# Kernel tuning notes

Hardware: AMD Instinct MI355X
Metric: run time of the kernel (lower is better)

## Reference

```python
import jax, jax.numpy as jnp
import numpy as np
from jax import lax

B, T, N_INPUT = 64, 2048, 257
HIDDEN = 32
N_OUTPUT = 10


def setup_inputs() -> dict:
    key = jax.random.key(0)
    ks = jax.random.split(key, 7)
    return {
        "specs": jax.random.normal(ks[0], (B, T, N_INPUT), dtype=jnp.float32),
        "W_ih": jax.random.normal(ks[1], (4 * HIDDEN, N_INPUT), dtype=jnp.float32) * 0.05,
        "W_hh": jax.random.normal(ks[2], (4 * HIDDEN, HIDDEN), dtype=jnp.float32) * 0.05,
        "b_ih": jax.random.normal(ks[3], (4 * HIDDEN,), dtype=jnp.float32) * 0.05,
        "b_hh": jax.random.normal(ks[4], (4 * HIDDEN,), dtype=jnp.float32) * 0.05,
        "W_out": jax.random.normal(ks[5], (N_OUTPUT, HIDDEN), dtype=jnp.float32) * 0.05,
        "b_out": jax.random.normal(ks[6], (N_OUTPUT,), dtype=jnp.float32) * 0.05,
    }


def reference(specs, W_ih, W_hh, b_ih, b_hh, W_out, b_out):
    # specs: [B, T, n_input]. PyTorch LSTMCell, gate order (i, f, g, o).
    b, t, _ = specs.shape
    h0 = jnp.zeros((b, HIDDEN), dtype=specs.dtype)
    c0 = jnp.zeros((b, HIDDEN), dtype=specs.dtype)
    # Precompute input projection for all timesteps in one GEMM: [B, T, 4H]
    x_proj = jnp.einsum("bti,gi->btg", specs, W_ih) + b_ih + b_hh
    x_proj = jnp.swapaxes(x_proj, 0, 1)  # [T, B, 4H] for scan

    def step(carry, xg):
        h, c = carry
        gates = xg + h @ W_hh.T  # [B, 4H]
        i, f, g, o = jnp.split(gates, 4, axis=-1)
        i = jax.nn.sigmoid(i)
        f = jax.nn.sigmoid(f)
        g = jnp.tanh(g)
        o = jax.nn.sigmoid(o)
        c = f * c + i * g
        h = o * jnp.tanh(c)
        return (h, c), None

    (hn, _), _ = lax.scan(step, (h0, c0), x_proj)
    logits = jax.nn.relu(hn) @ W_out.T + b_out  # [B, n_output]
    return jax.nn.log_softmax(logits, axis=1)
```

## Files before the change

kernel.cpp:

```cpp
#include <hip/hip_runtime.h>

#define B_SZ 64
#define T_LEN 2048
#define NIN 257
#define HID 32
#define G4 128
#define NOUT 10

#define TBT 128
#define PAD 34
#define CH 8
#define NSCAN 64
#define NGEMMP 128
#define NTILE 1024
#define TPB 16

typedef int v2i __attribute__((ext_vector_type(2)));
typedef unsigned long long u64;

__device__ __forceinline__ float fsig(float x) {
  return __builtin_amdgcn_rcpf(1.f + __builtin_amdgcn_exp2f(-1.44269504089f * x));
}

__device__ __forceinline__ void pkfma2(float2& acc, float2 w, u64 h2) {
  asm("v_pk_fma_f32 %0, %1, %2, %0" : "+v"(acc) : "v"(w), "s"(h2));
}

__device__ __forceinline__ void gemm_tile(
    const float* __restrict__ A, const float* __restrict__ W,
    const float* __restrict__ b_ih, const float* __restrict__ b_hh,
    float* __restrict__ C, int bt0, float* sA, float* sB)
{
  const int tid = threadIdx.x;
  const int gt = tid & 15;
  const int btt = tid >> 4;
  float acc[8][8];
#pragma unroll
  for (int i = 0; i < 8; ++i)
#pragma unroll
    for (int j = 0; j < 8; ++j) acc[i][j] = 0.f;

  for (int kc = 0; kc < 8; ++kc) {
    const int k0 = kc * 32;
    __syncthreads();
#pragma unroll
    for (int i = 0; i < 16; ++i) {
      int s = i * 256 + tid;
      int r = s >> 5, cc = s & 31;
      sA[r * PAD + cc] = A[(size_t)(bt0 + r) * NIN + k0 + cc];
      sB[r * PAD + cc] = W[(size_t)r * NIN + k0 + cc];
    }
    __syncthreads();
#pragma unroll
    for (int k2 = 0; k2 < 16; ++k2) {
      float2 a2[8], b2[8];
#pragma unroll
      for (int i = 0; i < 8; ++i)
        a2[i] = *(const float2*)&sA[(btt + 16 * i) * PAD + 2 * k2];
#pragma unroll
      for (int j = 0; j < 8; ++j)
        b2[j] = *(const float2*)&sB[(gt + 16 * j) * PAD + 2 * k2];
#pragma unroll
      for (int i = 0; i < 8; ++i)
#pragma unroll
        for (int j = 0; j < 8; ++j) {
          acc[i][j] = fmaf(a2[i].x, b2[j].x, acc[i][j]);
          acc[i][j] = fmaf(a2[i].y, b2[j].y, acc[i][j]);
        }
    }
  }
  {
    float a[8], bb[8];
#pragma unroll
    for (int i = 0; i < 8; ++i) a[i] = A[(size_t)(bt0 + btt + 16 * i) * NIN + 256];
#pragma unroll
    for (int j = 0; j < 8; ++j) bb[j] = W[(size_t)(gt + 16 * j) * NIN + 256];
#pragma unroll
    for (int i = 0; i < 8; ++i)
#pragma unroll
      for (int j = 0; j < 8; ++j) acc[i][j] += a[i] * bb[j];
  }
  float bias[8];
#pragma unroll
  for (int j = 0; j < 8; ++j) bias[j] = b_ih[gt + 16 * j] + b_hh[gt + 16 * j];
#pragma unroll
  for (int i = 0; i < 8; ++i) {
    size_t row = (size_t)(bt0 + btt + 16 * i) * G4;
#pragma unroll
    for (int j = 0; j < 8; ++j) C[row + gt + 16 * j] = acc[i][j] + bias[j];
  }
}

__global__ __launch_bounds__(256) void fused(
    const float* __restrict__ A,
    const float* __restrict__ W,
    const float* __restrict__ b_ih,
    const float* __restrict__ b_hh,
    const float* __restrict__ W_hh,
    const float* __restrict__ W_out,
    const float* __restrict__ b_out,
    float* __restrict__ out,
    float* __restrict__ xproj,
    int* __restrict__ flags,
    int nowait)
{
  __shared__ float sA[TBT * PAD];
  __shared__ float sB[G4 * PAD];
  const int bid = blockIdx.x;

  if (bid >= NSCAN) {
    const int p = bid - NSCAN;
    for (int idx = p; idx < NTILE; idx += NGEMMP) {
      const int ti = idx >> 6, bb = idx & 63;
      const int bt0 = bb * T_LEN + ti * TBT;
      gemm_tile(A, W, b_ih, b_hh, xproj, bt0, sA, sB);
      __threadfence();
      __syncthreads();
      if (threadIdx.x == 0)
        __hip_atomic_store(&flags[idx], 1, __ATOMIC_RELEASE, __HIP_MEMORY_SCOPE_AGENT);
    }
    return;
  }

  if (threadIdx.x >= 64) return;
  __builtin_amdgcn_s_setprio(3);
  const int b = bid;
  const int l = threadIdx.x;

  float2 wA[16], wB[16];
#pragma unroll
  for (int j = 0; j < 16; j += 2) {
    float4 v0 = *(const float4*)&W_hh[l * HID + 2 * j];
    wA[j]     = make_float2(v0.x, v0.y);
    wA[j + 1] = make_float2(v0.z, v0.w);
    float4 v1 = *(const float4*)&W_hh[(l + 64) * HID + 2 * j];
    wB[j]     = make_float2(v1.x, v1.y);
    wB[j + 1] = make_float2(v1.z, v1.w);
  }
  const float sBc = (l < HID) ? 2.f : 1.f;
  const float mBc = (l < HID) ? 2.f : 1.f;
  const float aBc = (l < HID) ? -1.f : 0.f;

  float c = 0.f, h = 0.f;
  u64 hp[16];
#pragma unroll
  for (int k = 0; k < 16; ++k) hp[k] = 0ull;

  const float* xb = xproj + (size_t)b * T_LEN * G4;

  auto step = [&](float xa, float xg) {
    float2 aA0 = make_float2(xa, 0.f), aA1 = make_float2(0.f, 0.f);
    float2 aB0 = make_float2(xg, 0.f), aB1 = make_float2(0.f, 0.f);
#pragma unroll
    for (int j = 0; j < 16; j += 2) {
      pkfma2(aA0, wA[j],     hp[j]);
      pkfma2(aA1, wA[j + 1], hp[j + 1]);
      pkfma2(aB0, wB[j],     hp[j]);
      pkfma2(aB1, wB[j + 1], hp[j + 1]);
    }
    float2 tA, tB;
    asm("v_pk_add_f32 %0, %1, %2" : "=v"(tA) : "v"(aA0), "v"(aA1));
    asm("v_pk_add_f32 %0, %1, %2" : "=v"(tB) : "v"(aB0), "v"(aB1));
    float accA = tA.x + tA.y;
    float accB = tB.x + tB.y;
    float actA = fsig(accA);
    float actB = mBc * fsig(accB * sBc) + aBc;
    float prod = actA * actB;
    v2i sw = __builtin_amdgcn_permlane32_swap(0, __float_as_int(prod), false, false);
    float pr = __int_as_float(sw[0]);
    c = fmaf(actA, c, pr);
    float th = 2.f * fsig(c + c) - 1.f;
    h = actB * th;
#pragma unroll
    for (int k = 0; k < 16; ++k) {
      unsigned lo = (unsigned)__builtin_amdgcn_readlane(__float_as_int(h), 32 + 2 * k);
      unsigned hi = (unsigned)__builtin_amdgcn_readlane(__float_as_int(h), 33 + 2 * k);
      hp[k] = (u64)lo | ((u64)hi << 32);
    }
  };

  for (int ti = 0; ti < TPB; ++ti) {
    if (!nowait) {
      while (__hip_atomic_load(&flags[ti * 64 + b], __ATOMIC_ACQUIRE,
                               __HIP_MEMORY_SCOPE_AGENT) == 0)
        __builtin_amdgcn_s_sleep(2);
    }
    const float* xt = xb + (size_t)ti * TBT * G4;
    float A0[CH], B0[CH], A1[CH], B1[CH];
#pragma unroll
    for (int i = 0; i < CH; ++i) {
      A0[i] = xt[i * G4 + l];
      B0[i] = xt[i * G4 + 64 + l];
    }
    for (int ch = 0; ch < TBT / CH; ch += 2) {
      const float* s1 = xt + (size_t)(ch + 1) * CH * G4;
#pragma unroll
      for (int i = 0; i < CH; ++i) {
        A1[i] = s1[i * G4 + l];
        B1[i] = s1[i * G4 + 64 + l];
      }
#pragma unroll
      for (int i = 0; i < CH; ++i) step(A0[i], B0[i]);
      if (ch + 2 < TBT / CH) {
        const float* s2 = xt + (size_t)(ch + 2) * CH * G4;
#pragma unroll
        for (int i = 0; i < CH; ++i) {
          A0[i] = s2[i * G4 + l];
          B0[i] = s2[i * G4 + 64 + l];
        }
      }
#pragma unroll
      for (int i = 0; i < CH; ++i) step(A1[i], B1[i]);
    }
  }

  float hf[HID];
#pragma unroll
  for (int k = 0; k < HID; ++k)
    hf[k] = __int_as_float(__builtin_amdgcn_readlane(__float_as_int(h), 32 + k));
  float logit = 0.f;
  if (l < NOUT) {
    logit = b_out[l];
#pragma unroll
    for (int j = 0; j < HID; ++j) logit += fmaxf(hf[j], 0.f) * W_out[l * HID + j];
  }
  float m = -1e30f;
#pragma unroll
  for (int n = 0; n < NOUT; ++n) m = fmaxf(m, __shfl(logit, n));
  float s = 0.f;
#pragma unroll
  for (int n = 0; n < NOUT; ++n)
    s += __builtin_amdgcn_exp2f(1.44269504089f * (__shfl(logit, n) - m));
  if (l < NOUT)
    out[b * NOUT + l] = logit - m - 0.69314718056f * __builtin_amdgcn_logf(s);
}

__global__ __launch_bounds__(256) void xproj_gemm(
    const float* __restrict__ A, const float* __restrict__ W,
    const float* __restrict__ b_ih, const float* __restrict__ b_hh,
    float* __restrict__ C)
{
  __shared__ float sA[TBT * PAD];
  __shared__ float sB[G4 * PAD];
  const int idx = blockIdx.x;
  const int ti = idx >> 6, bb = idx & 63;
  gemm_tile(A, W, b_ih, b_hh, C, bb * T_LEN + ti * TBT, sA, sB);
}

extern "C" void kernel_launch(void* const* d_in, const int* in_sizes, int n_in,
                              void* d_out, int out_size, void* d_ws, size_t ws_size,
                              hipStream_t stream) {
  const float* specs = (const float*)d_in[0];
  const float* W_ih  = (const float*)d_in[1];
  const float* W_hh  = (const float*)d_in[2];
  const float* b_ih  = (const float*)d_in[3];
  const float* b_hh  = (const float*)d_in[4];
  const float* W_out = (const float*)d_in[5];
  const float* b_out = (const float*)d_in[6];
  float* outp  = (float*)d_out;
  float* xproj = (float*)d_ws;
  const size_t xbytes = (size_t)B_SZ * T_LEN * G4 * 4;

  if (ws_size >= xbytes + NTILE * sizeof(int)) {
    int* flags = (int*)((char*)d_ws + xbytes);
    (void)hipMemsetAsync(flags, 0, NTILE * sizeof(int), stream);
    fused<<<NSCAN + NGEMMP, 256, 0, stream>>>(specs, W_ih, b_ih, b_hh, W_hh,
                                              W_out, b_out, outp, xproj, flags, 0);
  } else {
    xproj_gemm<<<NTILE, 256, 0, stream>>>(specs, W_ih, b_ih, b_hh, xproj);
    fused<<<NSCAN, 256, 0, stream>>>(specs, W_ih, b_ih, b_hh, W_hh,
                                     W_out, b_out, outp, xproj, (int*)xproj , 1);
  }
}
```

Before: 561.2 us.

## Split fused GEMM+scan into two kernels and widen recurrent FMA accumulator chains

Removes the flag-based producer/consumer overlap, where 128 GEMM blocks published tiles while 64 scan blocks polled flags. It now launches a standalone input-projection GEMM over all tiles, then a scan-only kernel with 64-thread blocks. The recurrent matvec now uses four packed accumulators per gate half instead of two, which shortens the dependent FMA chain on the serial critical path. The cost is that the GEMM no longer overlaps the scan, so the scan starts only after the whole projection finishes.

```diff
diff --git a/kernel.cpp b/kernel.cpp
--- a/kernel.cpp
+++ b/kernel.cpp
@@ -11,7 +11,6 @@
 #define PAD 34
 #define CH 8
 #define NSCAN 64
-#define NGEMMP 128
 #define NTILE 1024
 #define TPB 16
 
@@ -24,6 +23,12 @@
 
 __device__ __forceinline__ void pkfma2(float2& acc, float2 w, u64 h2) {
   asm("v_pk_fma_f32 %0, %1, %2, %0" : "+v"(acc) : "v"(w), "s"(h2));
+}
+
+__device__ __forceinline__ float2 pkadd(float2 a, float2 b) {
+  float2 d;
+  asm("v_pk_add_f32 %0, %1, %2" : "=v"(d) : "v"(a), "v"(b));
+  return d;
 }
 
 __device__ __forceinline__ void gemm_tile(
@@ -89,6 +94,18 @@
 #pragma unroll
     for (int j = 0; j < 8; ++j) C[row + gt + 16 * j] = acc[i][j] + bias[j];
   }
+}
+
+__global__ __launch_bounds__(256) void xproj_gemm(
+    const float* __restrict__ A, const float* __restrict__ W,
+    const float* __restrict__ b_ih, const float* __restrict__ b_hh,
+    float* __restrict__ C)
+{
+  __shared__ float sA[TBT * PAD];
+  __shared__ float sB[G4 * PAD];
+  const int idx = blockIdx.x;
+  const int ti = idx >> 6, bb = idx & 63;
+  gemm_tile(A, W, b_ih, b_hh, C, bb * T_LEN + ti * TBT, sA, sB);
 }
 
 __global__ __launch_bounds__(256) void fused(
@@ -104,24 +121,7 @@
     int* __restrict__ flags,
     int nowait)
 {
-  __shared__ float sA[TBT * PAD];
-  __shared__ float sB[G4 * PAD];
   const int bid = blockIdx.x;
-
-  if (bid >= NSCAN) {
-    const int p = bid - NSCAN;
-    for (int idx = p; idx < NTILE; idx += NGEMMP) {
-      const int ti = idx >> 6, bb = idx & 63;
-      const int bt0 = bb * T_LEN + ti * TBT;
-      gemm_tile(A, W, b_ih, b_hh, xproj, bt0, sA, sB);
-      __threadfence();
-      __syncthreads();
-      if (threadIdx.x == 0)
-        __hip_atomic_store(&flags[idx], 1, __ATOMIC_RELEASE, __HIP_MEMORY_SCOPE_AGENT);
-    }
-    return;
-  }
-
   if (threadIdx.x >= 64) return;
   __builtin_amdgcn_s_setprio(3);
   const int b = bid;
@@ -149,18 +149,24 @@
   const float* xb = xproj + (size_t)b * T_LEN * G4;
 
   auto step = [&](float xa, float xg) {
-    float2 aA0 = make_float2(xa, 0.f), aA1 = make_float2(0.f, 0.f);
-    float2 aB0 = make_float2(xg, 0.f), aB1 = make_float2(0.f, 0.f);
-#pragma unroll
-    for (int j = 0; j < 16; j += 2) {
-      pkfma2(aA0, wA[j],     hp[j]);
-      pkfma2(aA1, wA[j + 1], hp[j + 1]);
-      pkfma2(aB0, wB[j],     hp[j]);
-      pkfma2(aB1, wB[j + 1], hp[j + 1]);
-    }
-    float2 tA, tB;
-    asm("v_pk_add_f32 %0, %1, %2" : "=v"(tA) : "v"(aA0), "v"(aA1));
-    asm("v_pk_add_f32 %0, %1, %2" : "=v"(tB) : "v"(aB0), "v"(aB1));
+    float2 aA[4], aB[4];
+    aA[0] = make_float2(xa, 0.f);
+    aB[0] = make_float2(xg, 0.f);
+#pragma unroll
+    for (int q = 1; q < 4; ++q) {
+      aA[q] = make_float2(0.f, 0.f);
+      aB[q] = make_float2(0.f, 0.f);
+    }
+#pragma unroll
+    for (int j = 0; j < 16; j += 4) {
+#pragma unroll
+      for (int q = 0; q < 4; ++q) {
+        pkfma2(aA[q], wA[j + q], hp[j + q]);
+        pkfma2(aB[q], wB[j + q], hp[j + q]);
+      }
+    }
+    float2 tA = pkadd(pkadd(aA[0], aA[1]), pkadd(aA[2], aA[3]));
+    float2 tB = pkadd(pkadd(aB[0], aB[1]), pkadd(aB[2], aB[3]));
     float accA = tA.x + tA.y;
     float accB = tB.x + tB.y;
     float actA = fsig(accA);
@@ -233,18 +239,6 @@
     s += __builtin_amdgcn_exp2f(1.44269504089f * (__shfl(logit, n) - m));
   if (l < NOUT)
     out[b * NOUT + l] = logit - m - 0.69314718056f * __builtin_amdgcn_logf(s);
-}
-
-__global__ __launch_bounds__(256) void xproj_gemm(
-    const float* __restrict__ A, const float* __restrict__ W,
-    const float* __restrict__ b_ih, const float* __restrict__ b_hh,
-    float* __restrict__ C)
-{
-  __shared__ float sA[TBT * PAD];
-  __shared__ float sB[G4 * PAD];
-  const int idx = blockIdx.x;
-  const int ti = idx >> 6, bb = idx & 63;
-  gemm_tile(A, W, b_ih, b_hh, C, bb * T_LEN + ti * TBT, sA, sB);
 }
 
 extern "C" void kernel_launch(void* const* d_in, const int* in_sizes, int n_in,
@@ -259,16 +253,9 @@
   const float* b_out = (const float*)d_in[6];
   float* outp  = (float*)d_out;
   float* xproj = (float*)d_ws;
-  const size_t xbytes = (size_t)B_SZ * T_LEN * G4 * 4;
-
-  if (ws_size >= xbytes + NTILE * sizeof(int)) {
-    int* flags = (int*)((char*)d_ws + xbytes);
-    (void)hipMemsetAsync(flags, 0, NTILE * sizeof(int), stream);
-    fused<<<NSCAN + NGEMMP, 256, 0, stream>>>(specs, W_ih, b_ih, b_hh, W_hh,
-                                              W_out, b_out, outp, xproj, flags, 0);
-  } else {
-    xproj_gemm<<<NTILE, 256, 0, stream>>>(specs, W_ih, b_ih, b_hh, xproj);
-    fused<<<NSCAN, 256, 0, stream>>>(specs, W_ih, b_ih, b_hh, W_hh,
-                                     W_out, b_out, outp, xproj, (int*)xproj , 1);
-  }
-}
+
+  xproj_gemm<<<NTILE, 256, 0, stream>>>(specs, W_ih, b_ih, b_hh, xproj);
+  fused<<<NSCAN, 64, 0, stream>>>(specs, W_ih, b_ih, b_hh, W_hh,
+                                  W_out, b_out, outp, xproj,
+                                  (int*)xproj , 1 );
+}
```

Result: slower. 615.0 us (+9.6%).

## Hand-schedule xproj prefetch with inline asm loads and explicit vmcnt waits

Applied to the files above, without the earlier changes.

The recurrent scan loop now issues its x-projection loads as inline-asm global_load_dword pairs and uses explicit s_waitcnt vmcnt(16) waits with sched barriers. This keeps one chunk of loads in flight while the previous chunk is consumed, so the compiler cannot serialise or hoist the waits. The dot product over h is split into four independent packed-FMA accumulator chains instead of two, shortening the dependency chain on the serial critical path. The activations fold the scale constants into the exp2 argument and use fma for tanh. The hand-written asm and wait counts are fragile: any change in the number of other outstanding loads could make the waits wrong.

```diff
diff --git a/kernel.cpp b/kernel.cpp
--- a/kernel.cpp
+++ b/kernel.cpp
@@ -18,13 +18,36 @@
 typedef int v2i __attribute__((ext_vector_type(2)));
 typedef unsigned long long u64;
 
-__device__ __forceinline__ float fsig(float x) {
-  return __builtin_amdgcn_rcpf(1.f + __builtin_amdgcn_exp2f(-1.44269504089f * x));
-}
-
 __device__ __forceinline__ void pkfma2(float2& acc, float2 w, u64 h2) {
   asm("v_pk_fma_f32 %0, %1, %2, %0" : "+v"(acc) : "v"(w), "s"(h2));
 }
+
+__device__ __forceinline__ float2 pkadd(float2 a, float2 b) {
+  float2 d;
+  asm("v_pk_add_f32 %0, %1, %2" : "=v"(d) : "v"(a), "v"(b));
+  return d;
+}
+
+#define LDP(a0, b0, PB, OA, OB) \
+  asm volatile("global_load_dword %0, %2, off offset:" OA "\n\t" \
+               "global_load_dword %1, %2, off offset:" OB \
+               : "=&v"(a0), "=&v"(b0) : "v"(PB))
+
+#define LOAD_CHUNK(Aa, Bb, PB) do { \
+  LDP(Aa[0], Bb[0], PB, "0",    "256");  \
+  LDP(Aa[1], Bb[1], PB, "512",  "768");  \
+  LDP(Aa[2], Bb[2], PB, "1024", "1280"); \
+  LDP(Aa[3], Bb[3], PB, "1536", "1792"); \
+  LDP(Aa[4], Bb[4], PB, "2048", "2304"); \
+  LDP(Aa[5], Bb[5], PB, "2560", "2816"); \
+  LDP(Aa[6], Bb[6], PB, "3072", "3328"); \
+  LDP(Aa[7], Bb[7], PB, "3584", "3840"); \
+} while (0)
+
+#define WAIT16() do { asm volatile("s_waitcnt vmcnt(16)" ::: "memory"); \
+                      __builtin_amdgcn_sched_barrier(0); } while (0)
+#define WAIT0()  do { asm volatile("s_waitcnt vmcnt(0)" ::: "memory"); \
+                      __builtin_amdgcn_sched_barrier(0); } while (0)
 
 __device__ __forceinline__ void gemm_tile(
     const float* __restrict__ A, const float* __restrict__ W,
@@ -137,7 +160,7 @@
     wB[j]     = make_float2(v1.x, v1.y);
     wB[j + 1] = make_float2(v1.z, v1.w);
   }
-  const float sBc = (l < HID) ? 2.f : 1.f;
+  const float eB  = (l < HID) ? -2.88539008f : -1.44269504f;
   const float mBc = (l < HID) ? 2.f : 1.f;
   const float aBc = (l < HID) ? -1.f : 0.f;
 
@@ -149,28 +172,36 @@
   const float* xb = xproj + (size_t)b * T_LEN * G4;
 
   auto step = [&](float xa, float xg) {
-    float2 aA0 = make_float2(xa, 0.f), aA1 = make_float2(0.f, 0.f);
-    float2 aB0 = make_float2(xg, 0.f), aB1 = make_float2(0.f, 0.f);
-#pragma unroll
-    for (int j = 0; j < 16; j += 2) {
-      pkfma2(aA0, wA[j],     hp[j]);
-      pkfma2(aA1, wA[j + 1], hp[j + 1]);
-      pkfma2(aB0, wB[j],     hp[j]);
-      pkfma2(aB1, wB[j + 1], hp[j + 1]);
-    }
-    float2 tA, tB;
-    asm("v_pk_add_f32 %0, %1, %2" : "=v"(tA) : "v"(aA0), "v"(aA1));
-    asm("v_pk_add_f32 %0, %1, %2" : "=v"(tB) : "v"(aB0), "v"(aB1));
+    float2 aA[4], aB[4];
+    aA[0] = make_float2(xa, 0.f);
+    aB[0] = make_float2(xg, 0.f);
+#pragma unroll
+    for (int q = 1; q < 4; ++q) {
+      aA[q] = make_float2(0.f, 0.f);
+      aB[q] = make_float2(0.f, 0.f);
+    }
+#pragma unroll
+    for (int j = 0; j < 16; j += 4) {
+#pragma unroll
+      for (int q = 0; q < 4; ++q) {
+        pkfma2(aA[q], wA[j + q], hp[j + q]);
+        pkfma2(aB[q], wB[j + q], hp[j + q]);
+      }
+    }
+    float2 tA = pkadd(pkadd(aA[0], aA[1]), pkadd(aA[2], aA[3]));
+    float2 tB = pkadd(pkadd(aB[0], aB[1]), pkadd(aB[2], aB[3]));
     float accA = tA.x + tA.y;
     float accB = tB.x + tB.y;
-    float actA = fsig(accA);
-    float actB = mBc * fsig(accB * sBc) + aBc;
+    float actA = __builtin_amdgcn_rcpf(1.f + __builtin_amdgcn_exp2f(-1.44269504f * accA));
+    float sB2  = __builtin_amdgcn_rcpf(1.f + __builtin_amdgcn_exp2f(eB * accB));
+    float actB = fmaf(mBc, sB2, aBc);
     float prod = actA * actB;
     v2i sw = __builtin_amdgcn_permlane32_swap(0, __float_as_int(prod), false, false);
     float pr = __int_as_float(sw[0]);
     c = fmaf(actA, c, pr);
-    float th = 2.f * fsig(c + c) - 1.f;
-    h = actB * th;
+    float t  = __builtin_amdgcn_rcpf(1.f + __builtin_amdgcn_exp2f(-2.88539008f * c));
+    float o2 = actB + actB;
+    h = fmaf(o2, t, -actB);
 #pragma unroll
     for (int k = 0; k < 16; ++k) {
       unsigned lo = (unsigned)__builtin_amdgcn_readlane(__float_as_int(h), 32 + 2 * k);
@@ -178,6 +209,10 @@
       hp[k] = (u64)lo | ((u64)hi << 32);
     }
   };
+
+  float A0[CH], B0[CH], A1[CH], B1[CH];
+#define STEPS(Aa, Bb) do { _Pragma("unroll") \
+  for (int i = 0; i < CH; ++i) step(Aa[i], Bb[i]); } while (0)
 
   for (int ti = 0; ti < TPB; ++ti) {
     if (!nowait) {
@@ -185,33 +220,22 @@
                                __HIP_MEMORY_SCOPE_AGENT) == 0)
         __builtin_amdgcn_s_sleep(2);
     }
-    const float* xt = xb + (size_t)ti * TBT * G4;
-    float A0[CH], B0[CH], A1[CH], B1[CH];
-#pragma unroll
-    for (int i = 0; i < CH; ++i) {
-      A0[i] = xt[i * G4 + l];
-      B0[i] = xt[i * G4 + 64 + l];
-    }
-    for (int ch = 0; ch < TBT / CH; ch += 2) {
-      const float* s1 = xt + (size_t)(ch + 1) * CH * G4;
-#pragma unroll
-      for (int i = 0; i < CH; ++i) {
-        A1[i] = s1[i * G4 + l];
-        B1[i] = s1[i * G4 + 64 + l];
-      }
-#pragma unroll
-      for (int i = 0; i < CH; ++i) step(A0[i], B0[i]);
-      if (ch + 2 < TBT / CH) {
-        const float* s2 = xt + (size_t)(ch + 2) * CH * G4;
-#pragma unroll
-        for (int i = 0; i < CH; ++i) {
-          A0[i] = s2[i * G4 + l];
-          B0[i] = s2[i * G4 + 64 + l];
-        }
-      }
-#pragma unroll
-      for (int i = 0; i < CH; ++i) step(A1[i], B1[i]);
-    }
+    const float* pb = xb + (size_t)ti * TBT * G4 + l;
+    LOAD_CHUNK(A0, B0, pb); pb += CH * G4;
+    LOAD_CHUNK(A1, B1, pb); pb += CH * G4;
+#pragma unroll 1
+    for (int pc = 0; pc < 7; ++pc) {
+      WAIT16();
+      STEPS(A0, B0);
+      LOAD_CHUNK(A0, B0, pb); pb += CH * G4;
+      WAIT16();
+      STEPS(A1, B1);
+      LOAD_CHUNK(A1, B1, pb); pb += CH * G4;
+    }
+    WAIT16();
+    STEPS(A0, B0);
+    WAIT0();
+    STEPS(A1, B1);
   }
 
   float hf[HID];
```

Measured after the change: 571.8 us. Within noise of the previous version (+1.9%).
